# Performance work log

Hardware: AMD Instinct MI355X
Metric: run time of the kernel (lower is better)

The kernel has to match this reference:

```python
import jax, jax.numpy as jnp
import numpy as np

L = 128          # bandlimit (max_l)
NTHETA = 256     # Gauss-Legendre latitudes (>= L for exact quadrature)
NPHI = 512       # longitudes (>= 2L-1)
C_IN, C_OUT = 32, 32


def _normalized_assoc_legendre(Lmax, xg):
    """Pbar_lm(x) with Condon-Shortley phase, orthonormal on the sphere.
    Returns (Lmax, Lmax, T) for m>=0; zero for m>l."""
    T = xg.shape[0]
    P = np.zeros((Lmax, Lmax, T), dtype=np.float64)
    sx = np.sqrt(np.maximum(1.0 - xg * xg, 0.0))
    P[0, 0] = 1.0 / np.sqrt(4.0 * np.pi)
    for m in range(1, Lmax):
        P[m, m] = -np.sqrt((2 * m + 1) / (2.0 * m)) * sx * P[m - 1, m - 1]
    for m in range(0, Lmax - 1):
        P[m + 1, m] = np.sqrt(2 * m + 3.0) * xg * P[m, m]
    for m in range(Lmax):
        for l in range(m + 2, Lmax):
            a = np.sqrt((4.0 * l * l - 1.0) / (l * l - m * m))
            b = np.sqrt(((l - 1.0) ** 2 - m * m) / (4.0 * (l - 1.0) ** 2 - 1.0))
            P[l, m] = a * (xg * P[l - 1, m] - b * P[l - 2, m])
    return P


def _build_basis():
    # Gauss-Legendre quadrature in cos(theta): exact for degree <= 2*NTHETA-1
    xg, wg = np.polynomial.legendre.leggauss(NTHETA)
    P = _normalized_assoc_legendre(L, xg)  # (L, L, T), m>=0
    # Full basis B[l, m+L-1, t]; Pbar_{l,-m} = (-1)^m Pbar_{l,m}
    B = np.zeros((L, 2 * L - 1, NTHETA), dtype=np.float64)
    for m in range(-(L - 1), L):
        B[:, m + L - 1, :] = ((-1.0) ** abs(m) if m < 0 else 1.0) * P[:, abs(m), :]
    return B.astype(np.float32), wg.astype(np.float32)


def setup_inputs() -> dict:
    key = jax.random.key(0)
    k1, k2, k3 = jax.random.split(key, 3)
    x = jax.random.normal(k1, (NTHETA, NPHI, C_IN), dtype=jnp.float32)
    std = 1.0 / (C_IN + C_OUT)
    wr = std * jax.random.normal(k2, (L, 2 * L - 1, C_IN, C_OUT), dtype=jnp.float32)
    wi = std * jax.random.normal(k3, (L, 2 * L - 1, C_IN, C_OUT), dtype=jnp.float32)
    B, wg = _build_basis()
    return {"x": x, "weights_real": wr, "weights_imag": wi,
            "legendre": jnp.asarray(B), "quad_w": jnp.asarray(wg)}


def reference(x, weights_real, weights_imag, legendre, quad_w):
    ntheta, nphi, _ = x.shape
    Lb = legendre.shape[0]
    # --- forward SHT (per channel, vectorized) ---
    # longitude FFT: Fm[t,k,c] = sum_p x e^{-i 2pi k p / nphi}; dphi = 2pi/nphi
    Fm = jnp.fft.fft(x.astype(jnp.complex64), axis=1) * (2.0 * np.pi / nphi)
    midx = np.arange(-(Lb - 1), Lb) % nphi            # FFT bins for m=-(L-1)..L-1
    Fm_sel = Fm[:, midx, :]                           # (t, 2L-1, c)
    Bw = legendre * quad_w[None, None, :]             # quadrature-weighted basis
    # flm[l,m,c] = sum_t w_t Pbar_lm(theta_t) Fm[t,m,c]
    flm = jnp.einsum('lmt,tmc->lmc', Bw.astype(jnp.complex64), Fm_sel)
    # --- spectral conv: per-(l,m) channel mixing ---
    W = weights_real.astype(jnp.complex64) + 1j * weights_imag.astype(jnp.complex64)
    y = jnp.einsum('lmc,lmco->lmo', flm, W)           # (L, 2L-1, O)
    # --- inverse SHT ---
    G = jnp.einsum('lmt,lmo->tmo', legendre.astype(jnp.complex64), y)  # (t, 2L-1, O)
    spec = jnp.zeros((ntheta, nphi, G.shape[-1]), dtype=jnp.complex64)
    spec = spec.at[:, midx, :].set(G)
    out = jnp.fft.ifft(spec, axis=1) * nphi           # f = sum_m G e^{i m phi}
    return jnp.moveaxis(out.real, 2, 0)               # (O, ntheta, nphi)
```

## Files before the change

kernel.cpp:

```cpp
#include <hip/hip_runtime.h>
#include <math.h>

#define DEVFN __global__ __launch_bounds__(256)

namespace {
constexpr int LL  = 128;
constexpr int MM2 = 255;
constexpr int NT  = 256;
constexpr int NP  = 512;
constexpr int NC  = 32;
constexpr int NO  = 32;
constexpr float TWO_PI = 6.283185307179586476925286766559f;
}

typedef short v8s __attribute__((ext_vector_type(8)));
typedef float v4f __attribute__((ext_vector_type(4)));

__device__ inline unsigned short f2bf(float f) {
  unsigned int u = __float_as_uint(f);
  return (unsigned short)((u + 0x7FFFu + ((u >> 16) & 1u)) >> 16);
}

DEVFN void kp_prep(const float* __restrict__ x, unsigned short* __restrict__ tw1t,
                   unsigned short* __restrict__ vt, unsigned short* __restrict__ xb) {
  __shared__ float sm[32][65];
  const int bid = blockIdx.x;
  const int tid = threadIdx.x;
  const float phi = TWO_PI / (float)NP;
  if (bid < 512) {
    const int idx = bid * 256 + tid;
    const float fs = TWO_PI / (float)NP;
    {
      const int n = idx >> 9, p = idx & 511;
      const int m = n >> 1;
      const int k = (m * p) & (NP - 1);
      float s, c;
      sincosf(phi * (float)k, &s, &c);
      tw1t[idx] = f2bf((n & 1) ? (-s * fs) : (c * fs));
    }
    {
      const int p = idx >> 8, k = idx & 255;
      const int m = k >> 1;
      const int kk = (m * p) & (NP - 1);
      float s, c;
      sincosf(phi * (float)kk, &s, &c);
      vt[idx] = f2bf((k & 1) ? s : c);
    }
  } else {
    const int q = bid - 512;
    const int t = q >> 3;
    const int p0 = (q & 7) * 64;
#pragma unroll
    for (int i = 0; i < 8; ++i) {
      const int idx = tid + i * 256;
      const int p = idx >> 5, c = idx & 31;
      sm[c][p] = x[((size_t)t * NP + p0 + p) * NC + c];
    }
    __syncthreads();
    const int c = tid >> 3, pg = tid & 7;
    unsigned short pk[8];
#pragma unroll
    for (int u = 0; u < 8; ++u) pk[u] = f2bf(sm[c][pg * 8 + u]);
    *(uint4*)(xb + ((size_t)(t * 32 + c)) * NP + p0 + pg * 8) = *(const uint4*)pk;
  }
}

DEVFN void k1_mfma(const unsigned short* __restrict__ xb,
                   const unsigned short* __restrict__ tw1t,
                   const float* __restrict__ wg,
                   float* __restrict__ fwr, float* __restrict__ fwi) {
  __shared__ unsigned short As[128 * 32];
  __shared__ unsigned short Bs[128 * 32];
  const int tid = threadIdx.x;
  const int r0 = blockIdx.x * 128;
  const int n0 = blockIdx.y * 128;
  const int wid = tid >> 6, lane = tid & 63;
  const int wm = wid & 1, wn = wid >> 1;
  v4f acc[4][4];
#pragma unroll
  for (int i = 0; i < 4; ++i)
#pragma unroll
    for (int j = 0; j < 4; ++j) {
      acc[i][j][0] = 0.f; acc[i][j][1] = 0.f; acc[i][j][2] = 0.f; acc[i][j][3] = 0.f;
    }
  const int lr = lane & 15, lk = (lane >> 4) * 8;
  for (int k0 = 0; k0 < 512; k0 += 32) {
#pragma unroll
    for (int s = 0; s < 2; ++s) {
      const int chunk = tid + s * 256;
      const int row = chunk >> 2, c16 = chunk & 3;
      *(uint4*)&As[row * 32 + c16 * 8] =
          *(const uint4*)&xb[(size_t)(r0 + row) * 512 + k0 + c16 * 8];
      *(uint4*)&Bs[row * 32 + c16 * 8] =
          *(const uint4*)&tw1t[(size_t)(n0 + row) * 512 + k0 + c16 * 8];
    }
    __syncthreads();
    v8s af[4], bf[4];
#pragma unroll
    for (int i = 0; i < 4; ++i) af[i] = *(const v8s*)&As[(wm * 64 + i * 16 + lr) * 32 + lk];
#pragma unroll
    for (int j = 0; j < 4; ++j) bf[j] = *(const v8s*)&Bs[(wn * 64 + j * 16 + lr) * 32 + lk];
#pragma unroll
    for (int i = 0; i < 4; ++i)
#pragma unroll
      for (int j = 0; j < 4; ++j)
        acc[i][j] = __builtin_amdgcn_mfma_f32_16x16x32_bf16(af[i], bf[j], acc[i][j], 0, 0, 0);
    __syncthreads();
  }
  const int lrow = (lane >> 4) * 4;
#pragma unroll
  for (int i = 0; i < 4; ++i) {
    const int rbase = r0 + wm * 64 + i * 16 + lrow;
    const int t = rbase >> 5, c0 = rbase & 31;
    const float w = wg[t];
#pragma unroll
    for (int j = 0; j < 4; ++j) {
      const int n = n0 + wn * 64 + j * 16 + lr;
      const int mI = n >> 1;
      float* dst = (n & 1) ? fwi : fwr;
      float4 v = {acc[i][j][0] * w, acc[i][j][1] * w, acc[i][j][2] * w, acc[i][j][3] * w};
      *(float4*)&dst[((size_t)mI * NT + t) * NC + c0] = v;
    }
  }
}

DEVFN void k2_flm(const float* __restrict__ leg, const float* __restrict__ fwr,
                  const float* __restrict__ fwi, float* __restrict__ flr,
                  float* __restrict__ fli) {
  const int m = blockIdx.x;
  const int l = m + blockIdx.y * 8 + (threadIdx.x >> 5);
  const int c = threadIdx.x & 31;
  if (l >= LL) return;
  const float* lg = leg + ((size_t)(l * MM2 + 127 + m)) * NT;
  const float* fr = fwr + (size_t)m * NT * NC + c;
  const float* fi = fwi + (size_t)m * NT * NC + c;
  float ar = 0.f, ai = 0.f;
  for (int t = 0; t < NT; t += 4) {
    const float4 b4 = *(const float4*)(lg + t);
    ar = fmaf(b4.x, fr[(t + 0) * NC], ar);
    ai = fmaf(b4.x, fi[(t + 0) * NC], ai);
    ar = fmaf(b4.y, fr[(t + 1) * NC], ar);
    ai = fmaf(b4.y, fi[(t + 1) * NC], ai);
    ar = fmaf(b4.z, fr[(t + 2) * NC], ar);
    ai = fmaf(b4.z, fi[(t + 2) * NC], ai);
    ar = fmaf(b4.w, fr[(t + 3) * NC], ar);
    ai = fmaf(b4.w, fi[(t + 3) * NC], ai);
  }
  flr[(m * LL + l) * NC + c] = ar;
  fli[(m * LL + l) * NC + c] = ai;
}

DEVFN void k3_y(const float* __restrict__ wr, const float* __restrict__ wi,
                const float* __restrict__ flr, const float* __restrict__ fli,
                float* __restrict__ ya, float* __restrict__ yb) {
  const int m = blockIdx.x;
  const int wid = threadIdx.x >> 6;
  const int lane = threadIdx.x & 63;
  const int l = m + blockIdx.y * 4 + wid;
  if (l >= LL) return;
  const int oo = lane & 31;
  const int half = lane >> 5;
  const float s0 = (m > 0) ? 1.0f : 0.0f;
  const size_t bp = ((size_t)(l * MM2 + 127 + m) * NC) * NO + oo;
  const size_t bn = ((size_t)(l * MM2 + 127 - m) * NC) * NO + oo;
  const float* fr = flr + (size_t)(m * LL + l) * NC + half * 16;
  const float* fi = fli + (size_t)(m * LL + l) * NC + half * 16;
  float accA = 0.f, accB = 0.f;
#pragma unroll
  for (int u = 0; u < 16; ++u) {
    const size_t co = (size_t)(half * 16 + u) * NO;
    const float wrp = wr[bp + co];
    const float wrn = wr[bn + co];
    const float wip = wi[bp + co];
    const float win = wi[bn + co];
    const float fa = fr[u];
    const float fb = fi[u];
    const float wa = fmaf(s0, wrn, wrp);
    const float wb = fmaf(s0, win, -wip);
    accA = fmaf(fa, wa, fmaf(fb, wb, accA));
    accB = fmaf(fa, wb, fmaf(-fb, wa, accB));
  }
  accA += __shfl_down(accA, 32);
  accB += __shfl_down(accB, 32);
  if (lane < 32) {
    ya[(size_t)(m * LL + l) * NO + oo] = accA;
    yb[(size_t)(m * LL + l) * NO + oo] = accB;
  }
}

DEVFN void k4_G(const float* __restrict__ leg, const float* __restrict__ ya,
                const float* __restrict__ yb, unsigned short* __restrict__ ut) {
  const int m = blockIdx.x;
  const int o = threadIdx.x & 31;
  const int tq = threadIdx.x >> 5;
  const int t0 = blockIdx.y * 32 + tq * 4;
  float aa[4] = {}, bb[4] = {};
  for (int l = m; l < LL; ++l) {
    const float4 g = *(const float4*)(leg + ((size_t)(l * MM2 + 127 + m)) * NT + t0);
    const float yav = ya[(m * LL + l) * NO + o];
    const float ybv = yb[(m * LL + l) * NO + o];
    aa[0] = fmaf(g.x, yav, aa[0]);  bb[0] = fmaf(g.x, ybv, bb[0]);
    aa[1] = fmaf(g.y, yav, aa[1]);  bb[1] = fmaf(g.y, ybv, bb[1]);
    aa[2] = fmaf(g.z, yav, aa[2]);  bb[2] = fmaf(g.z, ybv, bb[2]);
    aa[3] = fmaf(g.w, yav, aa[3]);  bb[3] = fmaf(g.w, ybv, bb[3]);
  }
#pragma unroll
  for (int i = 0; i < 4; ++i) {
    const unsigned int pk = (unsigned int)f2bf(aa[i]) | ((unsigned int)f2bf(bb[i]) << 16);
    *(unsigned int*)&ut[((size_t)((t0 + i) * 32 + o)) * 256 + 2 * m] = pk;
  }
}

DEVFN void k5_mfma(const unsigned short* __restrict__ ut,
                   const unsigned short* __restrict__ vt,
                   float* __restrict__ out) {
  __shared__ unsigned short As[128 * 32];
  __shared__ unsigned short Bs[128 * 32];
  const int tid = threadIdx.x;
  const int p0 = blockIdx.x * 128;
  const int r0 = blockIdx.y * 128;
  const int wid = tid >> 6, lane = tid & 63;
  const int wm = wid & 1, wn = wid >> 1;
  v4f acc[4][4];
#pragma unroll
  for (int i = 0; i < 4; ++i)
#pragma unroll
    for (int j = 0; j < 4; ++j) {
      acc[i][j][0] = 0.f; acc[i][j][1] = 0.f; acc[i][j][2] = 0.f; acc[i][j][3] = 0.f;
    }
  const int lr = lane & 15, lk = (lane >> 4) * 8;
  for (int k0 = 0; k0 < 256; k0 += 32) {
#pragma unroll
    for (int s = 0; s < 2; ++s) {
      const int chunk = tid + s * 256;
      const int row = chunk >> 2, c16 = chunk & 3;
      *(uint4*)&As[row * 32 + c16 * 8] =
          *(const uint4*)&vt[(size_t)(p0 + row) * 256 + k0 + c16 * 8];
      *(uint4*)&Bs[row * 32 + c16 * 8] =
          *(const uint4*)&ut[(size_t)(r0 + row) * 256 + k0 + c16 * 8];
    }
    __syncthreads();
    v8s af[4], bf[4];
#pragma unroll
    for (int i = 0; i < 4; ++i) af[i] = *(const v8s*)&As[(wm * 64 + i * 16 + lr) * 32 + lk];
#pragma unroll
    for (int j = 0; j < 4; ++j) bf[j] = *(const v8s*)&Bs[(wn * 64 + j * 16 + lr) * 32 + lk];
#pragma unroll
    for (int i = 0; i < 4; ++i)
#pragma unroll
      for (int j = 0; j < 4; ++j)
        acc[i][j] = __builtin_amdgcn_mfma_f32_16x16x32_bf16(af[i], bf[j], acc[i][j], 0, 0, 0);
    __syncthreads();
  }
  const int lrow = (lane >> 4) * 4;
#pragma unroll
  for (int i = 0; i < 4; ++i) {
    const int pbase = p0 + wm * 64 + i * 16 + lrow;
#pragma unroll
    for (int j = 0; j < 4; ++j) {
      const int r = r0 + wn * 64 + j * 16 + lr;
      const int t = r >> 5, o = r & 31;
      float4 v = {acc[i][j][0], acc[i][j][1], acc[i][j][2], acc[i][j][3]};
      *(float4*)&out[((size_t)o * NT + t) * NP + pbase] = v;
    }
  }
}

extern "C" void kernel_launch(void* const* d_in, const int* in_sizes, int n_in,
                              void* d_out, int out_size, void* d_ws, size_t ws_size,
                              hipStream_t stream) {
  const float* x   = (const float*)d_in[0];
  const float* wr  = (const float*)d_in[1];
  const float* wi  = (const float*)d_in[2];
  const float* leg = (const float*)d_in[3];
  const float* wg  = (const float*)d_in[4];
  float* out = (float*)d_out;

  unsigned short* tw1t = (unsigned short*)d_ws;
  unsigned short* vt   = tw1t + 131072;
  unsigned short* xb   = vt + 131072;
  unsigned short* ut   = xb + 4194304;
  float* fwr = (float*)(ut + 2097152);
  float* fwi = fwr + 1048576;
  float* flr = fwi + 1048576;
  float* fli = flr + 524288;
  float* ya  = fli + 524288;
  float* yb  = ya + 524288;

  hipLaunchKernelGGL(kp_prep, dim3(2560), dim3(256), 0, stream, x, tw1t, vt, xb);
  hipLaunchKernelGGL(k1_mfma, dim3(64, 2), dim3(256), 0, stream, xb, tw1t, wg, fwr, fwi);
  hipLaunchKernelGGL(k2_flm, dim3(128, 16), dim3(256), 0, stream, leg, fwr, fwi, flr, fli);
  hipLaunchKernelGGL(k3_y, dim3(128, 32), dim3(256), 0, stream, wr, wi, flr, fli, ya, yb);
  hipLaunchKernelGGL(k4_G, dim3(128, 8), dim3(256), 0, stream, leg, ya, yb, ut);
  hipLaunchKernelGGL(k5_mfma, dim3(4, 64), dim3(256), 0, stream, ut, vt, out);
}
```

Baseline: 400.2 us.

## Fuse Legendre projection with channel mixing, retile forward DFT GEMM, remap block order

Merges the forward Legendre projection (k2) and the per-(l,m) channel-mixing kernel (k3) into one kernel. The flm coefficients now pass through shared memory instead of global buffers, which saves a launch and a global round trip. The forward DFT GEMM tile is halved in N to double its grid, for better CU occupancy. Both the fused kernel and k4 remap block indices so that work for different m values is spread across blocks, and k4's l-loop is unrolled. The fused kernel does half the work per thread on the projection, and its grid gives one wave per l, which may cost redundancy or efficiency.

```diff
diff --git a/kernel.cpp b/kernel.cpp
--- a/kernel.cpp
+++ b/kernel.cpp
@@ -70,40 +70,45 @@
                    const float* __restrict__ wg,
                    float* __restrict__ fwr, float* __restrict__ fwi) {
   __shared__ unsigned short As[128 * 32];
-  __shared__ unsigned short Bs[128 * 32];
+  __shared__ unsigned short Bs[64 * 32];
   const int tid = threadIdx.x;
   const int r0 = blockIdx.x * 128;
-  const int n0 = blockIdx.y * 128;
+  const int n0 = blockIdx.y * 64;
   const int wid = tid >> 6, lane = tid & 63;
   const int wm = wid & 1, wn = wid >> 1;
-  v4f acc[4][4];
+  v4f acc[4][2];
 #pragma unroll
   for (int i = 0; i < 4; ++i)
 #pragma unroll
-    for (int j = 0; j < 4; ++j) {
+    for (int j = 0; j < 2; ++j) {
       acc[i][j][0] = 0.f; acc[i][j][1] = 0.f; acc[i][j][2] = 0.f; acc[i][j][3] = 0.f;
     }
   const int lr = lane & 15, lk = (lane >> 4) * 8;
   for (int k0 = 0; k0 < 512; k0 += 32) {
 #pragma unroll
-    for (int s = 0; s < 2; ++s) {
+    for (int s = 0; s < 3; ++s) {
       const int chunk = tid + s * 256;
-      const int row = chunk >> 2, c16 = chunk & 3;
-      *(uint4*)&As[row * 32 + c16 * 8] =
-          *(const uint4*)&xb[(size_t)(r0 + row) * 512 + k0 + c16 * 8];
-      *(uint4*)&Bs[row * 32 + c16 * 8] =
-          *(const uint4*)&tw1t[(size_t)(n0 + row) * 512 + k0 + c16 * 8];
-    }
-    __syncthreads();
-    v8s af[4], bf[4];
+      if (chunk < 512) {
+        const int row = chunk >> 2, c16 = chunk & 3;
+        *(uint4*)&As[row * 32 + c16 * 8] =
+            *(const uint4*)&xb[(size_t)(r0 + row) * 512 + k0 + c16 * 8];
+      } else {
+        const int bc = chunk - 512;
+        const int row = bc >> 2, c16 = bc & 3;
+        *(uint4*)&Bs[row * 32 + c16 * 8] =
+            *(const uint4*)&tw1t[(size_t)(n0 + row) * 512 + k0 + c16 * 8];
+      }
+    }
+    __syncthreads();
+    v8s af[4], bf[2];
 #pragma unroll
     for (int i = 0; i < 4; ++i) af[i] = *(const v8s*)&As[(wm * 64 + i * 16 + lr) * 32 + lk];
 #pragma unroll
-    for (int j = 0; j < 4; ++j) bf[j] = *(const v8s*)&Bs[(wn * 64 + j * 16 + lr) * 32 + lk];
+    for (int j = 0; j < 2; ++j) bf[j] = *(const v8s*)&Bs[(wn * 32 + j * 16 + lr) * 32 + lk];
 #pragma unroll
     for (int i = 0; i < 4; ++i)
 #pragma unroll
-      for (int j = 0; j < 4; ++j)
+      for (int j = 0; j < 2; ++j)
         acc[i][j] = __builtin_amdgcn_mfma_f32_16x16x32_bf16(af[i], bf[j], acc[i][j], 0, 0, 0);
     __syncthreads();
   }
@@ -114,8 +119,8 @@
     const int t = rbase >> 5, c0 = rbase & 31;
     const float w = wg[t];
 #pragma unroll
-    for (int j = 0; j < 4; ++j) {
-      const int n = n0 + wn * 64 + j * 16 + lr;
+    for (int j = 0; j < 2; ++j) {
+      const int n = n0 + wn * 32 + j * 16 + lr;
       const int mI = n >> 1;
       float* dst = (n & 1) ? fwi : fwr;
       float4 v = {acc[i][j][0] * w, acc[i][j][1] * w, acc[i][j][2] * w, acc[i][j][3] * w};
@@ -124,47 +129,41 @@
   }
 }
 
-DEVFN void k2_flm(const float* __restrict__ leg, const float* __restrict__ fwr,
-                  const float* __restrict__ fwi, float* __restrict__ flr,
-                  float* __restrict__ fli) {
-  const int m = blockIdx.x;
-  const int l = m + blockIdx.y * 8 + (threadIdx.x >> 5);
-  const int c = threadIdx.x & 31;
-  if (l >= LL) return;
-  const float* lg = leg + ((size_t)(l * MM2 + 127 + m)) * NT;
-  const float* fr = fwr + (size_t)m * NT * NC + c;
-  const float* fi = fwi + (size_t)m * NT * NC + c;
-  float ar = 0.f, ai = 0.f;
-  for (int t = 0; t < NT; t += 4) {
-    const float4 b4 = *(const float4*)(lg + t);
-    ar = fmaf(b4.x, fr[(t + 0) * NC], ar);
-    ai = fmaf(b4.x, fi[(t + 0) * NC], ai);
-    ar = fmaf(b4.y, fr[(t + 1) * NC], ar);
-    ai = fmaf(b4.y, fi[(t + 1) * NC], ai);
-    ar = fmaf(b4.z, fr[(t + 2) * NC], ar);
-    ai = fmaf(b4.z, fi[(t + 2) * NC], ai);
-    ar = fmaf(b4.w, fr[(t + 3) * NC], ar);
-    ai = fmaf(b4.w, fi[(t + 3) * NC], ai);
-  }
-  flr[(m * LL + l) * NC + c] = ar;
-  fli[(m * LL + l) * NC + c] = ai;
-}
-
-DEVFN void k3_y(const float* __restrict__ wr, const float* __restrict__ wi,
-                const float* __restrict__ flr, const float* __restrict__ fli,
-                float* __restrict__ ya, float* __restrict__ yb) {
-  const int m = blockIdx.x;
-  const int wid = threadIdx.x >> 6;
-  const int lane = threadIdx.x & 63;
-  const int l = m + blockIdx.y * 4 + wid;
-  if (l >= LL) return;
+DEVFN void k23(const float* __restrict__ leg, const float* __restrict__ fwr,
+               const float* __restrict__ fwi, const float* __restrict__ wr,
+               const float* __restrict__ wi, float* __restrict__ ya,
+               float* __restrict__ yb) {
+  __shared__ float sf[4][64];
+  const int fid  = blockIdx.x + (int)blockIdx.y * 128;
+  const int wid4 = (fid & 7) * 512 + (fid >> 3);
+  const int m  = wid4 >> 5;
+  const int by = wid4 & 31;
+  const int wid = threadIdx.x >> 6, lane = threadIdx.x & 63;
+  const int l = m + by * 4 + wid;
+  const bool valid = (l < LL);
+  if (valid) {
+    const int c = lane & 31;
+    const float* lg = leg + ((size_t)(l * MM2 + 127 + m)) * NT;
+    const float* fp = ((lane >> 5) ? fwi : fwr) + (size_t)m * NT * NC + c;
+    float a = 0.f;
+    for (int t = 0; t < NT; t += 4) {
+      const float4 b4 = *(const float4*)(lg + t);
+      a = fmaf(b4.x, fp[(t + 0) * NC], a);
+      a = fmaf(b4.y, fp[(t + 1) * NC], a);
+      a = fmaf(b4.z, fp[(t + 2) * NC], a);
+      a = fmaf(b4.w, fp[(t + 3) * NC], a);
+    }
+    sf[wid][lane] = a;
+  }
+  __syncthreads();
+  if (!valid) return;
   const int oo = lane & 31;
   const int half = lane >> 5;
   const float s0 = (m > 0) ? 1.0f : 0.0f;
   const size_t bp = ((size_t)(l * MM2 + 127 + m) * NC) * NO + oo;
   const size_t bn = ((size_t)(l * MM2 + 127 - m) * NC) * NO + oo;
-  const float* fr = flr + (size_t)(m * LL + l) * NC + half * 16;
-  const float* fi = fli + (size_t)(m * LL + l) * NC + half * 16;
+  const float* fr = &sf[wid][half * 16];
+  const float* fi = &sf[wid][32 + half * 16];
   float accA = 0.f, accB = 0.f;
 #pragma unroll
   for (int u = 0; u < 16; ++u) {
@@ -190,11 +189,14 @@
 
 DEVFN void k4_G(const float* __restrict__ leg, const float* __restrict__ ya,
                 const float* __restrict__ yb, unsigned short* __restrict__ ut) {
-  const int m = blockIdx.x;
+  const int fid  = blockIdx.x + (int)blockIdx.y * 128;
+  const int wid4 = (fid & 7) * 128 + (fid >> 3);
+  const int m = wid4 >> 3;
   const int o = threadIdx.x & 31;
   const int tq = threadIdx.x >> 5;
-  const int t0 = blockIdx.y * 32 + tq * 4;
+  const int t0 = (wid4 & 7) * 32 + tq * 4;
   float aa[4] = {}, bb[4] = {};
+#pragma unroll 4
   for (int l = m; l < LL; ++l) {
     const float4 g = *(const float4*)(leg + ((size_t)(l * MM2 + 127 + m)) * NT + t0);
     const float yav = ya[(m * LL + l) * NO + o];
@@ -282,15 +284,12 @@
   unsigned short* ut   = xb + 4194304;
   float* fwr = (float*)(ut + 2097152);
   float* fwi = fwr + 1048576;
-  float* flr = fwi + 1048576;
-  float* fli = flr + 524288;
-  float* ya  = fli + 524288;
+  float* ya  = fwi + 1048576;
   float* yb  = ya + 524288;
 
   hipLaunchKernelGGL(kp_prep, dim3(2560), dim3(256), 0, stream, x, tw1t, vt, xb);
-  hipLaunchKernelGGL(k1_mfma, dim3(64, 2), dim3(256), 0, stream, xb, tw1t, wg, fwr, fwi);
-  hipLaunchKernelGGL(k2_flm, dim3(128, 16), dim3(256), 0, stream, leg, fwr, fwi, flr, fli);
-  hipLaunchKernelGGL(k3_y, dim3(128, 32), dim3(256), 0, stream, wr, wi, flr, fli, ya, yb);
+  hipLaunchKernelGGL(k1_mfma, dim3(64, 4), dim3(256), 0, stream, xb, tw1t, wg, fwr, fwi);
+  hipLaunchKernelGGL(k23, dim3(128, 32), dim3(256), 0, stream, leg, fwr, fwi, wr, wi, ya, yb);
   hipLaunchKernelGGL(k4_G, dim3(128, 8), dim3(256), 0, stream, leg, ya, yb, ut);
   hipLaunchKernelGGL(k5_mfma, dim3(4, 64), dim3(256), 0, stream, ut, vt, out);
 }
```

Measured after the change: 391.3 us. 2.2% less time.
